# Performance work log

Hardware: AMD Instinct MI355X
Metric: run time of the kernel (lower is better)

## Reference

```python
import jax, jax.numpy as jnp
import numpy as np

N_STREAMS = 4
HIDDEN = 1024
SINKHORN_ITERS = 20
TAU = 0.05
EPS = 1e-6
RMS_EPS = 1e-8


def rms_norm(x, weight):
    # x: [T, d] fp32
    rms = jnp.mean(x * x, axis=-1, keepdims=True)
    return x * jax.lax.rsqrt(rms + RMS_EPS) * weight


def sinkhorn_log(logits, n_iters=SINKHORN_ITERS, tau=TAU):
    # logits: [T, n, n] -> doubly-stochastic [T, n, n]
    Z = logits / tau
    u0 = jnp.zeros(Z.shape[:-1], Z.dtype)  # [T, n]
    v0 = jnp.zeros_like(u0)

    def body(i, uv):
        u, v = uv
        u = -jax.nn.logsumexp(Z + v[..., None, :], axis=-1)
        v = -jax.nn.logsumexp(Z + u[..., :, None], axis=-2)
        return (u, v)

    u, v = jax.lax.fori_loop(0, n_iters, body, (u0, v0))
    return jnp.exp(Z + u[..., :, None] + v[..., None, :])


def setup_inputs() -> dict:
    key = jax.random.key(0)
    ks = jax.random.split(key, 6)
    d = N_STREAMS * HIDDEN
    x_streams = jax.random.normal(ks[0], (4, 2048, N_STREAMS, HIDDEN), dtype=jnp.float32)
    scale = 1.0 / np.sqrt(d)
    return {
        "x_streams": x_streams,
        "rms_weight": jnp.ones((d,), jnp.float32),
        "W_pre": jax.random.normal(ks[1], (N_STREAMS, d), jnp.float32) * scale,
        "W_post": jax.random.normal(ks[2], (N_STREAMS, d), jnp.float32) * scale,
        "W_res": jax.random.normal(ks[3], (N_STREAMS * N_STREAMS, d), jnp.float32) * scale,
        "bias_pre": jnp.zeros((N_STREAMS,), jnp.float32),
        "bias_post": jnp.zeros((N_STREAMS,), jnp.float32),
        "bias_res": jnp.zeros((N_STREAMS * N_STREAMS,), jnp.float32),
        "alpha_pre": jnp.full((1,), 0.01, jnp.float32),
        "alpha_post": jnp.full((1,), 0.01, jnp.float32),
        "alpha_res": jnp.full((1,), 0.01, jnp.float32),
        "W_sub": jax.random.normal(ks[4], (HIDDEN, HIDDEN), jnp.float32) * (1.0 / np.sqrt(HIDDEN)),
    }


def reference(x_streams, rms_weight, W_pre, W_post, W_res, bias_pre, bias_post,
              bias_res, alpha_pre, alpha_post, alpha_res, W_sub):
    B, S, n, C = x_streams.shape
    d = n * C
    x_flat = x_streams.reshape(B * S, d).astype(jnp.float32)
    x_norm = rms_norm(x_flat, rms_weight)

    H_pre = jax.nn.sigmoid(alpha_pre * (x_norm @ W_pre.T) + bias_pre)        # [T, n]
    H_post = 2.0 * jax.nn.sigmoid(alpha_post * (x_norm @ W_post.T) + bias_post)
    H_res = sinkhorn_log((alpha_res * (x_norm @ W_res.T) + bias_res).reshape(B * S, n, n))

    H_pre = H_pre.reshape(B, S, n)
    H_post = H_post.reshape(B, S, n)
    H_res = H_res.reshape(B, S, n, n)

    H_pre_w = H_pre / (jnp.sum(H_pre, axis=-1, keepdims=True) + EPS)
    H_post_w = H_post / (jnp.sum(H_post, axis=-1, keepdims=True) + EPS)

    # pre-aggregate streams -> single stream
    x_layer = jnp.einsum('bsnc,bsn->bsc', x_streams, H_pre_w)
    # sublayer: bias-free linear
    y = x_layer @ W_sub.T                                                    # [B, S, C]
    # broadcast sublayer output back to streams
    y_expanded = H_post_w[..., None] * y[:, :, None, :]                      # [B, S, n, C]
    # doubly-stochastic residual stream mixing
    x_mixed = jnp.einsum('bsic,bsoi->bsoc', x_streams, H_res)
    return x_mixed + y_expanded
```

## Files before the change

kernel.cpp:

```cpp
#include <hip/hip_runtime.h>

#define NTOK 8192
#define D 4096
#define CH 1024

typedef __attribute__((ext_vector_type(8))) short short8v;
typedef __attribute__((ext_vector_type(4))) float float4v;
typedef __attribute__((ext_vector_type(4))) unsigned short ushort4v;

static __device__ __forceinline__ unsigned short f2bf(float f) {
  unsigned int u = __float_as_uint(f);
  u += 0x7fff + ((u >> 16) & 1);
  return (unsigned short)(u >> 16);
}

static __device__ __forceinline__ void async_cp16(const void* g, void* l) {
  __builtin_amdgcn_global_load_lds((__attribute__((address_space(1))) void*)g,
                                   (__attribute__((address_space(3))) void*)l,
                                   16, 0, 0);
}

__global__ __launch_bounds__(256) void prep_wsub(const float* __restrict__ Wsub,
                                                 unsigned short* __restrict__ Wb) {
  int i = blockIdx.x * 256 + threadIdx.x;
  float4 v = ((const float4*)Wsub)[i];
  ushort4v o;
  o.x = f2bf(v.x); o.y = f2bf(v.y); o.z = f2bf(v.z); o.w = f2bf(v.w);
  ((ushort4v*)Wb)[i] = o;
}

__global__ __launch_bounds__(256) void gates_kernel(
    const float* __restrict__ x, const float* __restrict__ rms_w,
    const float* __restrict__ Wpre, const float* __restrict__ Wpost,
    const float* __restrict__ Wres, const float* __restrict__ bpre,
    const float* __restrict__ bpost, const float* __restrict__ bres,
    const float* __restrict__ apre, const float* __restrict__ apost,
    const float* __restrict__ ares, float* __restrict__ gates_out,
    unsigned short* __restrict__ xlayer) {
  __shared__ float xbuf[8][256];
  __shared__ float logits_lds[8][24];
  __shared__ float sq_lds[8];
  __shared__ float hpre_lds[8][4];

  const int tid = threadIdx.x;
  const int lane = tid & 63;
  const int w = tid >> 6;
  const int tok0 = blockIdx.x * 8;

  const float* Wp[6];
#pragma unroll
  for (int g = 0; g < 6; ++g) {
    int gg = w * 6 + g;
    Wp[g] = (gg < 4) ? (Wpre + gg * D)
          : (gg < 8) ? (Wpost + (gg - 4) * D)
                     : (Wres + (gg - 8) * D);
  }

  float acc[6][8];
#pragma unroll
  for (int g = 0; g < 6; ++g)
#pragma unroll
    for (int t = 0; t < 8; ++t) acc[g][t] = 0.f;
  float sq0 = 0.f, sq1 = 0.f;

  for (int chk = 0; chk < 16; ++chk) {
    const int cb = chk * 256;
#pragma unroll
    for (int r = 0; r < 2; ++r) {
      int id = tid + r * 256;
      int t = id >> 6, j = id & 63;
      float4 v = *(const float4*)(x + (size_t)(tok0 + t) * D + cb + j * 4);
      *(float4*)(&xbuf[t][j * 4]) = v;
    }
    __syncthreads();
    float4 w4[6];
#pragma unroll
    for (int g = 0; g < 6; ++g) w4[g] = *(const float4*)(Wp[g] + cb + lane * 4);
    float4 r4 = *(const float4*)(rms_w + cb + lane * 4);
#pragma unroll
    for (int t = 0; t < 8; ++t) {
      float4 xv = *(const float4*)(&xbuf[t][lane * 4]);
      float ss = xv.x * xv.x + xv.y * xv.y + xv.z * xv.z + xv.w * xv.w;
      if ((t >> 1) == w) { if (t & 1) sq1 += ss; else sq0 += ss; }
      float4 xr;
      xr.x = xv.x * r4.x; xr.y = xv.y * r4.y; xr.z = xv.z * r4.z; xr.w = xv.w * r4.w;
#pragma unroll
      for (int g = 0; g < 6; ++g)
        acc[g][t] += xr.x * w4[g].x + xr.y * w4[g].y + xr.z * w4[g].z + xr.w * w4[g].w;
    }
    __syncthreads();
  }

#pragma unroll
  for (int g = 0; g < 6; ++g)
#pragma unroll
    for (int t = 0; t < 8; ++t) {
      float v = acc[g][t];
      for (int off = 32; off > 0; off >>= 1) v += __shfl_xor(v, off, 64);
      if (lane == 0) logits_lds[t][w * 6 + g] = v;
    }
  {
    float v0 = sq0, v1 = sq1;
    for (int off = 32; off > 0; off >>= 1) {
      v0 += __shfl_xor(v0, off, 64);
      v1 += __shfl_xor(v1, off, 64);
    }
    if (lane == 0) { sq_lds[w * 2] = v0; sq_lds[w * 2 + 1] = v1; }
  }
  __syncthreads();

  if (tid < 8) {
    const int t = tid;
    const int token = tok0 + t;
    float s = rsqrtf(sq_lds[t] * (1.0f / 4096.0f) + 1e-8f);
    float a_pre = apre[0], a_post = apost[0], a_res = ares[0];

    float hp[4];
    float sum_p = 1e-6f;
#pragma unroll
    for (int i = 0; i < 4; ++i) {
      float z = a_pre * (s * logits_lds[t][i]) + bpre[i];
      hp[i] = 1.0f / (1.0f + __expf(-z));
      sum_p += hp[i];
    }
    float inv_p = 1.0f / sum_p;
#pragma unroll
    for (int i = 0; i < 4; ++i) hpre_lds[t][i] = hp[i] * inv_p;

    float* go = gates_out + (size_t)token * 20;
    float hq[4];
    float sum_q = 1e-6f;
#pragma unroll
    for (int i = 0; i < 4; ++i) {
      float z = a_post * (s * logits_lds[t][4 + i]) + bpost[i];
      hq[i] = 2.0f / (1.0f + __expf(-z));
      sum_q += hq[i];
    }
    float inv_q = 1.0f / sum_q;
#pragma unroll
    for (int i = 0; i < 4; ++i) go[i] = hq[i] * inv_q;

    float Zm[16];
#pragma unroll
    for (int j = 0; j < 16; ++j)
      Zm[j] = (a_res * (s * logits_lds[t][8 + j]) + bres[j]) * 20.0f;
    float u[4] = {0, 0, 0, 0}, v[4] = {0, 0, 0, 0};
    for (int it = 0; it < 20; ++it) {
#pragma unroll
      for (int r = 0; r < 4; ++r) {
        float a0 = Zm[r * 4 + 0] + v[0], a1 = Zm[r * 4 + 1] + v[1];
        float a2 = Zm[r * 4 + 2] + v[2], a3 = Zm[r * 4 + 3] + v[3];
        float m = fmaxf(fmaxf(a0, a1), fmaxf(a2, a3));
        float sm = __expf(a0 - m) + __expf(a1 - m) + __expf(a2 - m) + __expf(a3 - m);
        u[r] = -(m + __logf(sm));
      }
#pragma unroll
      for (int c = 0; c < 4; ++c) {
        float a0 = Zm[0 + c] + u[0], a1 = Zm[4 + c] + u[1];
        float a2 = Zm[8 + c] + u[2], a3 = Zm[12 + c] + u[3];
        float m = fmaxf(fmaxf(a0, a1), fmaxf(a2, a3));
        float sm = __expf(a0 - m) + __expf(a1 - m) + __expf(a2 - m) + __expf(a3 - m);
        v[c] = -(m + __logf(sm));
      }
    }
#pragma unroll
    for (int r = 0; r < 4; ++r)
#pragma unroll
      for (int c = 0; c < 4; ++c)
        go[4 + r * 4 + c] = __expf(Zm[r * 4 + c] + u[r] + v[c]);
  }
  __syncthreads();

#pragma unroll
  for (int t = 0; t < 8; ++t) {
    float h0 = hpre_lds[t][0], h1 = hpre_lds[t][1];
    float h2 = hpre_lds[t][2], h3 = hpre_lds[t][3];
    const size_t base = (size_t)(tok0 + t) * D;
    float4 x0 = *(const float4*)(x + base + 0 * CH + tid * 4);
    float4 x1 = *(const float4*)(x + base + 1 * CH + tid * 4);
    float4 x2 = *(const float4*)(x + base + 2 * CH + tid * 4);
    float4 x3 = *(const float4*)(x + base + 3 * CH + tid * 4);
    ushort4v o;
    o.x = f2bf(h0 * x0.x + h1 * x1.x + h2 * x2.x + h3 * x3.x);
    o.y = f2bf(h0 * x0.y + h1 * x1.y + h2 * x2.y + h3 * x3.y);
    o.z = f2bf(h0 * x0.z + h1 * x1.z + h2 * x2.z + h3 * x3.z);
    o.w = f2bf(h0 * x0.w + h1 * x1.w + h2 * x2.w + h3 * x3.w);
    *(ushort4v*)(xlayer + (size_t)(tok0 + t) * CH + tid * 4) = o;
  }
}

__global__ __launch_bounds__(256) void gemm_epi(
    const unsigned short* __restrict__ A,
    const unsigned short* __restrict__ B,
    const float* __restrict__ x,
    const float* __restrict__ gates,
    float* __restrict__ out) {
  __shared__ unsigned short Asm[128 * 64];
  __shared__ unsigned short Bsm[128 * 64];
  __shared__ float gsm[128 * 20];

  const int tid = threadIdx.x;
  const int lane = tid & 63;
  const int w = tid >> 6;
  const int n0 = blockIdx.x * 128;
  const int m0 = blockIdx.y * 128;

  for (int i = tid; i < 128 * 20; i += 256) gsm[i] = gates[(size_t)m0 * 20 + i];

  float4v accf[4][4];
#pragma unroll
  for (int mi = 0; mi < 4; ++mi)
#pragma unroll
    for (int ni = 0; ni < 4; ++ni) {
      accf[mi][ni].x = 0.f; accf[mi][ni].y = 0.f;
      accf[mi][ni].z = 0.f; accf[mi][ni].w = 0.f;
    }

  const int wm = (w >> 1) * 64;
  const int wn = (w & 1) * 64;
  const int srow = lane >> 3;
  const int sslot = lane & 7;

  for (int kt = 0; kt < 16; ++kt) {
    const int k0 = kt * 64;
#pragma unroll
    for (int i = 0; i < 4; ++i) {
      int chunk = w * 4 + i;
      int row = chunk * 8 + srow;
      int qg = sslot ^ (row & 7);
      async_cp16(A + (size_t)(m0 + row) * 1024 + k0 + qg * 8,
                 (void*)(Asm + chunk * 512));
      async_cp16(B + (size_t)(n0 + row) * 1024 + k0 + qg * 8,
                 (void*)(Bsm + chunk * 512));
    }
    __syncthreads();
#pragma unroll
    for (int kk = 0; kk < 2; ++kk) {
      short8v a[4], b[4];
#pragma unroll
      for (int mi = 0; mi < 4; ++mi) {
        int row = wm + mi * 16 + (lane & 15);
        int q = (kk * 4 + (lane >> 4)) ^ (row & 7);
        a[mi] = *(const short8v*)(Asm + row * 64 + q * 8);
      }
#pragma unroll
      for (int ni = 0; ni < 4; ++ni) {
        int row = wn + ni * 16 + (lane & 15);
        int q = (kk * 4 + (lane >> 4)) ^ (row & 7);
        b[ni] = *(const short8v*)(Bsm + row * 64 + q * 8);
      }
#pragma unroll
      for (int mi = 0; mi < 4; ++mi)
#pragma unroll
        for (int ni = 0; ni < 4; ++ni)
          accf[mi][ni] = __builtin_amdgcn_mfma_f32_16x16x32_bf16(
              a[mi], b[ni], accf[mi][ni], 0, 0, 0);
    }
    __syncthreads();
  }

#pragma unroll
  for (int mi = 0; mi < 4; ++mi) {
#pragma unroll
    for (int ni = 0; ni < 4; ++ni) {
      const int ch = n0 + wn + ni * 16 + (lane & 15);
#pragma unroll
      for (int r = 0; r < 4; ++r) {
        const int tl = wm + mi * 16 + (lane >> 4) * 4 + r;
        const size_t t = (size_t)(m0 + tl);
        const float* gp = gsm + tl * 20;
        const size_t xb = t * 4096 + ch;
        float x0 = x[xb], x1 = x[xb + 1024], x2 = x[xb + 2048], x3 = x[xb + 3072];
        float y = accf[mi][ni][r];
#pragma unroll
        for (int o = 0; o < 4; ++o) {
          float res = x0 * gp[4 + o * 4 + 0] + x1 * gp[4 + o * 4 + 1] +
                      x2 * gp[4 + o * 4 + 2] + x3 * gp[4 + o * 4 + 3] +
                      gp[o] * y;
          out[t * 4096 + (size_t)o * 1024 + ch] = res;
        }
      }
    }
  }
}

extern "C" void kernel_launch(void* const* d_in, const int* in_sizes, int n_in,
                              void* d_out, int out_size, void* d_ws, size_t ws_size,
                              hipStream_t stream) {
  const float* x     = (const float*)d_in[0];
  const float* rms_w = (const float*)d_in[1];
  const float* Wpre  = (const float*)d_in[2];
  const float* Wpost = (const float*)d_in[3];
  const float* Wres  = (const float*)d_in[4];
  const float* bpre  = (const float*)d_in[5];
  const float* bpost = (const float*)d_in[6];
  const float* bres  = (const float*)d_in[7];
  const float* apre  = (const float*)d_in[8];
  const float* apost = (const float*)d_in[9];
  const float* ares  = (const float*)d_in[10];
  const float* Wsub  = (const float*)d_in[11];
  float* out = (float*)d_out;

  char* ws = (char*)d_ws;
  float* gates           = (float*)ws;
  unsigned short* Wb     = (unsigned short*)(ws + (1 << 20));
  unsigned short* xlayer = (unsigned short*)(ws + (4 << 20));

  prep_wsub<<<1024, 256, 0, stream>>>(Wsub, Wb);
  gates_kernel<<<1024, 256, 0, stream>>>(x, rms_w, Wpre, Wpost, Wres, bpre,
                                         bpost, bres, apre, apost, ares,
                                         gates, xlayer);
  gemm_epi<<<dim3(8, 64), 256, 0, stream>>>(xlayer, Wb, x, gates, out);
}
```

Before: 427.1 us.

## Double-buffer loads, parallelize Sinkhorn across lanes, vectorize GEMM epilogue via LDS

```diff
diff --git a/kernel.cpp b/kernel.cpp
--- a/kernel.cpp
+++ b/kernel.cpp
@@ -37,9 +37,10 @@
     const float* __restrict__ apre, const float* __restrict__ apost,
     const float* __restrict__ ares, float* __restrict__ gates_out,
     unsigned short* __restrict__ xlayer) {
-  __shared__ float xbuf[8][256];
+  __shared__ float xbuf[2][8][256];
   __shared__ float logits_lds[8][24];
   __shared__ float sq_lds[8];
+  __shared__ float s_lds[8];
   __shared__ float hpre_lds[8][4];
 
   const int tid = threadIdx.x;
@@ -63,23 +64,27 @@
     for (int t = 0; t < 8; ++t) acc[g][t] = 0.f;
   float sq0 = 0.f, sq1 = 0.f;
 
+  async_cp16(x + (size_t)(tok0 + 2 * w) * D + lane * 4, (void*)&xbuf[0][2 * w][0]);
+  async_cp16(x + (size_t)(tok0 + 2 * w + 1) * D + lane * 4, (void*)&xbuf[0][2 * w + 1][0]);
+  __syncthreads();
+
   for (int chk = 0; chk < 16; ++chk) {
     const int cb = chk * 256;
-#pragma unroll
-    for (int r = 0; r < 2; ++r) {
-      int id = tid + r * 256;
-      int t = id >> 6, j = id & 63;
-      float4 v = *(const float4*)(x + (size_t)(tok0 + t) * D + cb + j * 4);
-      *(float4*)(&xbuf[t][j * 4]) = v;
-    }
-    __syncthreads();
+    const int cur = chk & 1;
+    if (chk < 15) {
+      const int nb = cb + 256;
+      async_cp16(x + (size_t)(tok0 + 2 * w) * D + nb + lane * 4,
+                 (void*)&xbuf[cur ^ 1][2 * w][0]);
+      async_cp16(x + (size_t)(tok0 + 2 * w + 1) * D + nb + lane * 4,
+                 (void*)&xbuf[cur ^ 1][2 * w + 1][0]);
+    }
     float4 w4[6];
 #pragma unroll
     for (int g = 0; g < 6; ++g) w4[g] = *(const float4*)(Wp[g] + cb + lane * 4);
     float4 r4 = *(const float4*)(rms_w + cb + lane * 4);
 #pragma unroll
     for (int t = 0; t < 8; ++t) {
-      float4 xv = *(const float4*)(&xbuf[t][lane * 4]);
+      float4 xv = *(const float4*)(&xbuf[cur][t][lane * 4]);
       float ss = xv.x * xv.x + xv.y * xv.y + xv.z * xv.z + xv.w * xv.w;
       if ((t >> 1) == w) { if (t & 1) sq1 += ss; else sq0 += ss; }
       float4 xr;
@@ -111,9 +116,9 @@
 
   if (tid < 8) {
     const int t = tid;
-    const int token = tok0 + t;
     float s = rsqrtf(sq_lds[t] * (1.0f / 4096.0f) + 1e-8f);
-    float a_pre = apre[0], a_post = apost[0], a_res = ares[0];
+    s_lds[t] = s;
+    float a_pre = apre[0], a_post = apost[0];
 
     float hp[4];
     float sum_p = 1e-6f;
@@ -127,7 +132,7 @@
 #pragma unroll
     for (int i = 0; i < 4; ++i) hpre_lds[t][i] = hp[i] * inv_p;
 
-    float* go = gates_out + (size_t)token * 20;
+    float* go = gates_out + (size_t)(tok0 + t) * 20;
     float hq[4];
     float sum_q = 1e-6f;
 #pragma unroll
@@ -139,35 +144,6 @@
     float inv_q = 1.0f / sum_q;
 #pragma unroll
     for (int i = 0; i < 4; ++i) go[i] = hq[i] * inv_q;
-
-    float Zm[16];
-#pragma unroll
-    for (int j = 0; j < 16; ++j)
-      Zm[j] = (a_res * (s * logits_lds[t][8 + j]) + bres[j]) * 20.0f;
-    float u[4] = {0, 0, 0, 0}, v[4] = {0, 0, 0, 0};
-    for (int it = 0; it < 20; ++it) {
-#pragma unroll
-      for (int r = 0; r < 4; ++r) {
-        float a0 = Zm[r * 4 + 0] + v[0], a1 = Zm[r * 4 + 1] + v[1];
-        float a2 = Zm[r * 4 + 2] + v[2], a3 = Zm[r * 4 + 3] + v[3];
-        float m = fmaxf(fmaxf(a0, a1), fmaxf(a2, a3));
-        float sm = __expf(a0 - m) + __expf(a1 - m) + __expf(a2 - m) + __expf(a3 - m);
-        u[r] = -(m + __logf(sm));
-      }
-#pragma unroll
-      for (int c = 0; c < 4; ++c) {
-        float a0 = Zm[0 + c] + u[0], a1 = Zm[4 + c] + u[1];
-        float a2 = Zm[8 + c] + u[2], a3 = Zm[12 + c] + u[3];
-        float m = fmaxf(fmaxf(a0, a1), fmaxf(a2, a3));
-        float sm = __expf(a0 - m) + __expf(a1 - m) + __expf(a2 - m) + __expf(a3 - m);
-        v[c] = -(m + __logf(sm));
-      }
-    }
-#pragma unroll
-    for (int r = 0; r < 4; ++r)
-#pragma unroll
-      for (int c = 0; c < 4; ++c)
-        go[4 + r * 4 + c] = __expf(Zm[r * 4 + c] + u[r] + v[c]);
   }
   __syncthreads();
 
@@ -187,6 +163,42 @@
     o.w = f2bf(h0 * x0.w + h1 * x1.w + h2 * x2.w + h3 * x3.w);
     *(ushort4v*)(xlayer + (size_t)(tok0 + t) * CH + tid * 4) = o;
   }
+
+  if (tid < 32) {
+    const int t = tid >> 2;
+    const int r = tid & 3;
+    const float s = s_lds[t];
+    const float a_res = ares[0];
+    float Zrow[4], Zcol[4];
+#pragma unroll
+    for (int j = 0; j < 4; ++j) {
+      Zrow[j] = (a_res * (s * logits_lds[t][8 + r * 4 + j]) + bres[r * 4 + j]) * 20.0f;
+      Zcol[j] = (a_res * (s * logits_lds[t][8 + j * 4 + r]) + bres[j * 4 + r]) * 20.0f;
+    }
+    float u = 0.f, v = 0.f;
+    const int base = t << 2;
+    for (int it = 0; it < 20; ++it) {
+      float v0 = __shfl(v, base + 0, 64), v1 = __shfl(v, base + 1, 64);
+      float v2 = __shfl(v, base + 2, 64), v3 = __shfl(v, base + 3, 64);
+      float a0 = Zrow[0] + v0, a1 = Zrow[1] + v1, a2 = Zrow[2] + v2, a3 = Zrow[3] + v3;
+      float m = fmaxf(fmaxf(a0, a1), fmaxf(a2, a3));
+      float sm = __expf(a0 - m) + __expf(a1 - m) + __expf(a2 - m) + __expf(a3 - m);
+      u = -(m + __logf(sm));
+      float u0 = __shfl(u, base + 0, 64), u1 = __shfl(u, base + 1, 64);
+      float u2 = __shfl(u, base + 2, 64), u3 = __shfl(u, base + 3, 64);
+      float b0 = Zcol[0] + u0, b1 = Zcol[1] + u1, b2 = Zcol[2] + u2, b3 = Zcol[3] + u3;
+      float m2 = fmaxf(fmaxf(b0, b1), fmaxf(b2, b3));
+      float sm2 = __expf(b0 - m2) + __expf(b1 - m2) + __expf(b2 - m2) + __expf(b3 - m2);
+      v = -(m2 + __logf(sm2));
+    }
+    float v0 = __shfl(v, base + 0, 64), v1 = __shfl(v, base + 1, 64);
+    float v2 = __shfl(v, base + 2, 64), v3 = __shfl(v, base + 3, 64);
+    float* go = gates_out + (size_t)(tok0 + t) * 20;
+    go[4 + r * 4 + 0] = __expf(Zrow[0] + u + v0);
+    go[4 + r * 4 + 1] = __expf(Zrow[1] + u + v1);
+    go[4 + r * 4 + 2] = __expf(Zrow[2] + u + v2);
+    go[4 + r * 4 + 3] = __expf(Zrow[3] + u + v3);
+  }
 }
 
 __global__ __launch_bounds__(256) void gemm_epi(
@@ -195,9 +207,10 @@
     const float* __restrict__ x,
     const float* __restrict__ gates,
     float* __restrict__ out) {
-  __shared__ unsigned short Asm[128 * 64];
-  __shared__ unsigned short Bsm[128 * 64];
+  __shared__ __align__(16) char lds_raw[128 * 132 * 4];
   __shared__ float gsm[128 * 20];
+  unsigned short* stg = (unsigned short*)lds_raw;
+  float* ybuf = (float*)lds_raw;
 
   const int tid = threadIdx.x;
   const int lane = tid & 63;
@@ -221,19 +234,31 @@
   const int srow = lane >> 3;
   const int sslot = lane & 7;
 
+#define STAGE(KT, BUF)                                                        \
+  {                                                                           \
+    const int k0s = (KT) * 64;                                                \
+    unsigned short* As = stg + (BUF) * 8192;                                  \
+    unsigned short* Bs = stg + 16384 + (BUF) * 8192;                          \
+    _Pragma("unroll")                                                         \
+    for (int i = 0; i < 4; ++i) {                                             \
+      int chunk = w * 4 + i;                                                  \
+      int row = chunk * 8 + srow;                                             \
+      int qg = sslot ^ (row & 7);                                             \
+      async_cp16(A + (size_t)(m0 + row) * 1024 + k0s + qg * 8,                \
+                 (void*)(As + chunk * 512));                                  \
+      async_cp16(B + (size_t)(n0 + row) * 1024 + k0s + qg * 8,                \
+                 (void*)(Bs + chunk * 512));                                  \
+    }                                                                         \
+  }
+
+  STAGE(0, 0);
+  __syncthreads();
+
   for (int kt = 0; kt < 16; ++kt) {
-    const int k0 = kt * 64;
-#pragma unroll
-    for (int i = 0; i < 4; ++i) {
-      int chunk = w * 4 + i;
-      int row = chunk * 8 + srow;
-      int qg = sslot ^ (row & 7);
-      async_cp16(A + (size_t)(m0 + row) * 1024 + k0 + qg * 8,
-                 (void*)(Asm + chunk * 512));
-      async_cp16(B + (size_t)(n0 + row) * 1024 + k0 + qg * 8,
-                 (void*)(Bsm + chunk * 512));
-    }
-    __syncthreads();
+    const int cur = kt & 1;
+    if (kt < 15) STAGE(kt + 1, cur ^ 1);
+    const unsigned short* As = stg + cur * 8192;
+    const unsigned short* Bs = stg + 16384 + cur * 8192;
 #pragma unroll
     for (int kk = 0; kk < 2; ++kk) {
       short8v a[4], b[4];
@@ -241,13 +266,13 @@
       for (int mi = 0; mi < 4; ++mi) {
         int row = wm + mi * 16 + (lane & 15);
         int q = (kk * 4 + (lane >> 4)) ^ (row & 7);
-        a[mi] = *(const short8v*)(Asm + row * 64 + q * 8);
+        a[mi] = *(const short8v*)(As + row * 64 + q * 8);
       }
 #pragma unroll
       for (int ni = 0; ni < 4; ++ni) {
         int row = wn + ni * 16 + (lane & 15);
         int q = (kk * 4 + (lane >> 4)) ^ (row & 7);
-        b[ni] = *(const short8v*)(Bsm + row * 64 + q * 8);
+        b[ni] = *(const short8v*)(Bs + row * 64 + q * 8);
       }
 #pragma unroll
       for (int mi = 0; mi < 4; ++mi)
@@ -260,26 +285,41 @@
   }
 
 #pragma unroll
-  for (int mi = 0; mi < 4; ++mi) {
-#pragma unroll
-    for (int ni = 0; ni < 4; ++ni) {
-      const int ch = n0 + wn + ni * 16 + (lane & 15);
+  for (int mi = 0; mi < 4; ++mi)
+#pragma unroll
+    for (int ni = 0; ni < 4; ++ni)
 #pragma unroll
       for (int r = 0; r < 4; ++r) {
-        const int tl = wm + mi * 16 + (lane >> 4) * 4 + r;
-        const size_t t = (size_t)(m0 + tl);
-        const float* gp = gsm + tl * 20;
-        const size_t xb = t * 4096 + ch;
-        float x0 = x[xb], x1 = x[xb + 1024], x2 = x[xb + 2048], x3 = x[xb + 3072];
-        float y = accf[mi][ni][r];
-#pragma unroll
-        for (int o = 0; o < 4; ++o) {
-          float res = x0 * gp[4 + o * 4 + 0] + x1 * gp[4 + o * 4 + 1] +
-                      x2 * gp[4 + o * 4 + 2] + x3 * gp[4 + o * 4 + 3] +
-                      gp[o] * y;
-          out[t * 4096 + (size_t)o * 1024 + ch] = res;
-        }
+        int row = wm + mi * 16 + (lane >> 4) * 4 + r;
+        int col = wn + ni * 16 + (lane & 15);
+        ybuf[row * 132 + col] = accf[mi][ni][r];
       }
+  __syncthreads();
+
+#pragma unroll 4
+  for (int i = 0; i < 16; ++i) {
+    int idx = i * 256 + tid;
+    int tl = idx >> 5;
+    int c4 = idx & 31;
+    const size_t t = (size_t)(m0 + tl);
+    const float* gp = gsm + tl * 20;
+    float4 y4 = *(const float4*)&ybuf[tl * 132 + c4 * 4];
+    const size_t xb = t * 4096 + n0 + c4 * 4;
+    float4 x0 = *(const float4*)(x + xb);
+    float4 x1 = *(const float4*)(x + xb + 1024);
+    float4 x2 = *(const float4*)(x + xb + 2048);
+    float4 x3 = *(const float4*)(x + xb + 3072);
+#pragma unroll
+    for (int o = 0; o < 4; ++o) {
+      float h0 = gp[4 + o * 4 + 0], h1 = gp[4 + o * 4 + 1];
+      float h2 = gp[4 + o * 4 + 2], h3 = gp[4 + o * 4 + 3];
+      float hp = gp[o];
+      float4 rr;
+      rr.x = x0.x * h0 + x1.x * h1 + x2.x * h2 + x3.x * h3 + hp * y4.x;
+      rr.y = x0.y * h0 + x1.y * h1 + x2.y * h2 + x3.y * h3 + hp * y4.y;
+      rr.z = x0.z * h0 + x1.z * h1 + x2.z * h2 + x3.z * h3 + hp * y4.z;
+      rr.w = x0.w * h0 + x1.w * h1 + x2.w * h2 + x3.w * h3 + hp * y4.w;
+      *(float4*)(out + t * 4096 + (size_t)o * 1024 + n0 + c4 * 4) = rr;
     }
   }
 }
```

Result: no change. 424.6 us (-0.6%).
